# Kernel optimization log

Hardware: AMD Instinct MI355X
Metric: run time of the kernel (lower is better)

The kernel has to match this reference:

```python
import jax, jax.numpy as jnp
import numpy as np

POOL_SIZE = (14, 14)  # from init_kwargs


def setup_inputs() -> dict:
    key = jax.random.key(0)
    k1, k2 = jax.random.split(key)
    feature = jax.random.normal(k1, (1, 50, 50, 1024), dtype=jnp.float32)
    # rois in original-image coordinates [y1, x1, y2, x2], image is 800x800
    raw = jax.random.uniform(k2, (512, 4), dtype=jnp.float32) * 800.0
    y1 = jnp.minimum(raw[:, 0], raw[:, 2])
    y2 = jnp.maximum(raw[:, 0], raw[:, 2])
    x1 = jnp.minimum(raw[:, 1], raw[:, 3])
    x2 = jnp.maximum(raw[:, 1], raw[:, 3])
    rois = jnp.stack([y1, x1, y2, x2], axis=1)
    img_size = jnp.array([800, 800], dtype=jnp.int32)
    return {"feature": feature, "rois": rois, "img_size": img_size}


def _crop_and_resize(image, boxes, crop_size):
    """Faithful jax port of tf.image.crop_and_resize (bilinear, single image,
    all box_ind == 0). image: [1,H,W,C]; boxes: [N,4] normalized [y1,x1,y2,x2]."""
    H, W = image.shape[1], image.shape[2]
    ch, cw = crop_size
    img = image[0]  # [H, W, C]
    y1, x1, y2, x2 = boxes[:, 0], boxes[:, 1], boxes[:, 2], boxes[:, 3]
    # Sample grid in source-image pixel coordinates (TF convention: corners map
    # to box corners scaled by (dim-1)).
    ty = jnp.arange(ch, dtype=boxes.dtype) / (ch - 1)  # [ch]
    tx = jnp.arange(cw, dtype=boxes.dtype) / (cw - 1)  # [cw]
    ys = (y1[:, None] + ty[None, :] * (y2 - y1)[:, None]) * (H - 1)  # [N, ch]
    xs = (x1[:, None] + tx[None, :] * (x2 - x1)[:, None]) * (W - 1)  # [N, cw]
    y0f = jnp.floor(ys)
    x0f = jnp.floor(xs)
    wy = ys - y0f  # [N, ch] bilinear weights
    wx = xs - x0f  # [N, cw]
    y0 = jnp.clip(y0f, 0, H - 1).astype(jnp.int32)
    y1i = jnp.clip(y0f + 1, 0, H - 1).astype(jnp.int32)
    x0 = jnp.clip(x0f, 0, W - 1).astype(jnp.int32)
    x1i = jnp.clip(x0f + 1, 0, W - 1).astype(jnp.int32)

    def gather(yi, xi):  # [N,ch],[N,cw] -> [N,ch,cw,C]
        return img[yi[:, :, None], xi[:, None, :]]

    wxb = wx[:, None, :, None]  # [N,1,cw,1]
    wyb = wy[:, :, None, None]  # [N,ch,1,1]
    top = gather(y0, x0) * (1.0 - wxb) + gather(y0, x1i) * wxb
    bot = gather(y1i, x0) * (1.0 - wxb) + gather(y1i, x1i) * wxb
    return top * (1.0 - wyb) + bot * wyb  # [N, ch, cw, C]


def reference(feature, rois, img_size):
    h = img_size[0].astype(jnp.float32)
    w = img_size[1].astype(jnp.float32)
    normalization = jnp.stack([h, w, h, w], axis=0)
    boxes = rois / normalization
    return _crop_and_resize(feature, boxes, POOL_SIZE)
```

## Files before the change

kernel.cpp:

```cpp
#include <hip/hip_runtime.h>


#define FH 50
#define FW 50
#define FC 1024
#define PH 14
#define PW 14
#define CS 64
#define NSL (FC / CS)
#define QS (CS / 4)

typedef float f32x4 __attribute__((ext_vector_type(4)));

__global__ __launch_bounds__(256) void roi_crop_resize_kernel(
    const float* __restrict__ feat,
    const float* __restrict__ rois,
    const int* __restrict__ img_size,
    float* __restrict__ out)
{
    int bid = blockIdx.x;
    int n = bid >> 4;
    int s = bid & (NSL - 1);
    int t = threadIdx.x;
    int q = t & 15;
    int j = t >> 4;

    float hs = (float)img_size[0];
    float ws = (float)img_size[1];
    float by1 = rois[n * 4 + 0] / hs;
    float bx1 = rois[n * 4 + 1] / ws;
    float by2 = rois[n * 4 + 2] / hs;
    float bx2 = rois[n * 4 + 3] / ws;

    float ybase = by1 * (float)(FH - 1);
    float dy    = (by2 - by1) * (float)(FH - 1) * (1.0f / (float)(PH - 1));
    float xbase = bx1 * (float)(FW - 1);
    float dxs   = (bx2 - bx1) * (float)(FW - 1) * (1.0f / (float)(PW - 1));

    float xs  = xbase + (float)j * dxs;
    float x0f = floorf(xs);
    float wx  = xs - x0f;
    int x0 = (int)fminf(fmaxf(x0f,        0.0f), (float)(FW - 1));
    int x1 = (int)fminf(fmaxf(x0f + 1.0f, 0.0f), (float)(FW - 1));
    float omwx = 1.0f - wx;

    const f32x4* fq = (const f32x4*)feat;
    int sq = s * QS + q;
    f32x4* ob = (f32x4*)out + ((size_t)n * (PH * PW)) * (FC / 4) + sq;

    bool active = (j < PW);

    #pragma unroll
    for (int i = 0; i < PH; ++i) {
        float ysf = ybase + (float)i * dy;
        float y0f = floorf(ysf);
        float wy  = ysf - y0f;
        int r0 = (int)fminf(fmaxf(y0f,        0.0f), (float)(FH - 1));
        int r1 = (int)fminf(fmaxf(y0f + 1.0f, 0.0f), (float)(FH - 1));
        float omwy = 1.0f - wy;

        if (active) {
            int bT = (r0 * FW) * (FC / 4) + sq;
            int bB = (r1 * FW) * (FC / 4) + sq;
            f32x4 a = fq[bT + x0 * (FC / 4)];
            f32x4 b = fq[bT + x1 * (FC / 4)];
            f32x4 c = fq[bB + x0 * (FC / 4)];
            f32x4 d = fq[bB + x1 * (FC / 4)];

            f32x4 res = (a * omwx + b * wx) * omwy + (c * omwx + d * wx) * wy;

            __builtin_nontemporal_store(res, ob + (i * PW + j) * (FC / 4));
        }
    }
}

extern "C" void kernel_launch(void* const* d_in, const int* in_sizes, int n_in,
                              void* d_out, int out_size, void* d_ws, size_t ws_size,
                              hipStream_t stream) {
    const float* feat     = (const float*)d_in[0];
    const float* rois     = (const float*)d_in[1];
    const int*   img_size = (const int*)d_in[2];
    float* out = (float*)d_out;

    int n_rois = in_sizes[1] / 4;
    int grid   = n_rois * NSL;

    roi_crop_resize_kernel<<<grid, 256, 0, stream>>>(feat, rois, img_size, out);
}
```

Baseline: 80.71 us.

## Widen channel slice to 256 and assign two output columns per thread

Each block now covers 256 channels with 448 threads (7 column groups of 64 lanes), and each thread handles two output columns. Before, 256 threads covered 16 columns of 16 lanes, so 2 of those columns were idle. The change removes that idle work and makes each wavefront read 1 KB contiguous rows. It also cuts the grid to a quarter as many blocks, which lowers block-level parallelism and may affect occupancy.

```diff
diff --git a/kernel.cpp b/kernel.cpp
--- a/kernel.cpp
+++ b/kernel.cpp
@@ -6,24 +6,24 @@
 #define FC 1024
 #define PH 14
 #define PW 14
-#define CS 64
+#define CS 256
 #define NSL (FC / CS)
 #define QS (CS / 4)
 
 typedef float f32x4 __attribute__((ext_vector_type(4)));
 
-__global__ __launch_bounds__(256) void roi_crop_resize_kernel(
+__global__ __launch_bounds__(448) void roi_crop_resize_kernel(
     const float* __restrict__ feat,
     const float* __restrict__ rois,
     const int* __restrict__ img_size,
     float* __restrict__ out)
 {
     int bid = blockIdx.x;
-    int n = bid >> 4;
+    int n = bid >> 2;
     int s = bid & (NSL - 1);
     int t = threadIdx.x;
-    int q = t & 15;
-    int j = t >> 4;
+    int q = t & 63;
+    int g = t >> 6;
 
     float hs = (float)img_size[0];
     float ws = (float)img_size[1];
@@ -37,18 +37,21 @@
     float xbase = bx1 * (float)(FW - 1);
     float dxs   = (bx2 - bx1) * (float)(FW - 1) * (1.0f / (float)(PW - 1));
 
-    float xs  = xbase + (float)j * dxs;
-    float x0f = floorf(xs);
-    float wx  = xs - x0f;
-    int x0 = (int)fminf(fmaxf(x0f,        0.0f), (float)(FW - 1));
-    int x1 = (int)fminf(fmaxf(x0f + 1.0f, 0.0f), (float)(FW - 1));
-    float omwx = 1.0f - wx;
+    int   x0[2], x1[2];
+    float wx[2];
+    #pragma unroll
+    for (int jc = 0; jc < 2; ++jc) {
+        int j = jc * 7 + g;
+        float xs  = xbase + (float)j * dxs;
+        float x0f = floorf(xs);
+        wx[jc] = xs - x0f;
+        x0[jc] = (int)fminf(fmaxf(x0f,        0.0f), (float)(FW - 1));
+        x1[jc] = (int)fminf(fmaxf(x0f + 1.0f, 0.0f), (float)(FW - 1));
+    }
 
     const f32x4* fq = (const f32x4*)feat;
     int sq = s * QS + q;
-    f32x4* ob = (f32x4*)out + ((size_t)n * (PH * PW)) * (FC / 4) + sq;
-
-    bool active = (j < PW);
+    f32x4* ob = (f32x4*)out + (size_t)(n * (PH * PW)) * (FC / 4) + sq;
 
     #pragma unroll
     for (int i = 0; i < PH; ++i) {
@@ -58,16 +61,20 @@
         int r0 = (int)fminf(fmaxf(y0f,        0.0f), (float)(FH - 1));
         int r1 = (int)fminf(fmaxf(y0f + 1.0f, 0.0f), (float)(FH - 1));
         float omwy = 1.0f - wy;
+        int bT = (r0 * FW) * (FC / 4) + sq;
+        int bB = (r1 * FW) * (FC / 4) + sq;
 
-        if (active) {
-            int bT = (r0 * FW) * (FC / 4) + sq;
-            int bB = (r1 * FW) * (FC / 4) + sq;
-            f32x4 a = fq[bT + x0 * (FC / 4)];
-            f32x4 b = fq[bT + x1 * (FC / 4)];
-            f32x4 c = fq[bB + x0 * (FC / 4)];
-            f32x4 d = fq[bB + x1 * (FC / 4)];
+        #pragma unroll
+        for (int jc = 0; jc < 2; ++jc) {
+            int j = jc * 7 + g;
+            f32x4 a = fq[bT + x0[jc] * (FC / 4)];
+            f32x4 b = fq[bT + x1[jc] * (FC / 4)];
+            f32x4 c = fq[bB + x0[jc] * (FC / 4)];
+            f32x4 d = fq[bB + x1[jc] * (FC / 4)];
 
-            f32x4 res = (a * omwx + b * wx) * omwy + (c * omwx + d * wx) * wy;
+            float w  = wx[jc];
+            float ow = 1.0f - w;
+            f32x4 res = (a * ow + b * w) * omwy + (c * ow + d * w) * wy;
 
             __builtin_nontemporal_store(res, ob + (i * PW + j) * (FC / 4));
         }
@@ -85,5 +92,5 @@
     int n_rois = in_sizes[1] / 4;
     int grid   = n_rois * NSL;
 
-    roi_crop_resize_kernel<<<grid, 256, 0, stream>>>(feat, rois, img_size, out);
+    roi_crop_resize_kernel<<<grid, 448, 0, stream>>>(feat, rois, img_size, out);
 }
```

Result: no change. 82.15 us (+1.8%).
